# Kernel optimization log

Measured on AMD Instinct MI355X. Metric: run time of the kernel, lower is better.

Reference implementation:

```python
import jax, jax.numpy as jnp
import numpy as np

N, E, D, H, C = 50000, 800000, 128, 4, 32  # nodes, edges, embed dim, heads, head dim


def setup_inputs() -> dict:
    key = jax.random.key(0)
    ks = jax.random.split(key, 9)
    s = 1.0 / np.sqrt(D)
    return {
        "edge_index": jax.random.randint(ks[0], (2, E), 0, N),
        "emb": jax.random.normal(ks[1], (N, D), dtype=jnp.float32) * s,
        "W1": jax.random.normal(ks[2], (D, H * C), dtype=jnp.float32) * s,
        "att_src1": jax.random.normal(ks[3], (H, C), dtype=jnp.float32) * s,
        "att_dst1": jax.random.normal(ks[4], (H, C), dtype=jnp.float32) * s,
        "b1": jnp.zeros((H * C,), dtype=jnp.float32),
        "W2": jax.random.normal(ks[5], (D, D), dtype=jnp.float32) * s,
        "att_src2": jax.random.normal(ks[6], (1, D), dtype=jnp.float32) * s,
        "att_dst2": jax.random.normal(ks[7], (1, D), dtype=jnp.float32) * s,
        "b2": jnp.zeros((D,), dtype=jnp.float32),
    }


def _gat_conv(x, src, dst, W, a_src, a_dst, b, concat):
    """PyG-style GATConv: edge attention logits, segment softmax over dst, scatter-add."""
    n = x.shape[0]
    h, c = a_src.shape
    xl = (x @ W).reshape(n, h, c)                    # [N,H,C]
    a_s = (xl * a_src).sum(-1)                        # [N,H]
    a_d = (xl * a_dst).sum(-1)                        # [N,H]
    logits = jax.nn.leaky_relu(a_s[src] + a_d[dst], negative_slope=0.2)  # [E2,H]
    m = jax.ops.segment_max(logits, dst, num_segments=n)                 # per-dst max
    e = jnp.exp(logits - m[dst])
    denom = jax.ops.segment_sum(e, dst, num_segments=n)
    alpha = e / (denom[dst] + 1e-16)                  # [E2,H]
    msg = xl[src] * alpha[:, :, None]                 # [E2,H,C]
    out = jax.ops.segment_sum(msg, dst, num_segments=n)  # [N,H,C]
    out = out.reshape(n, h * c) if concat else out.mean(axis=1)
    return out + b


def reference(edge_index, emb, W1, att_src1, att_dst1, b1, W2, att_src2, att_dst2, b2):
    n = emb.shape[0]
    loop = jnp.arange(n)  # GATConv default add_self_loops=True
    src = jnp.concatenate([edge_index[0], loop])
    dst = jnp.concatenate([edge_index[1], loop])
    x = _gat_conv(emb, src, dst, W1, att_src1, att_dst1, b1, True)
    x = jax.nn.elu(x)
    x = _gat_conv(x, src, dst, W2, att_src2, att_dst2, b2, False)
    return x / jnp.maximum(jnp.linalg.norm(x, axis=1, keepdims=True), 1e-12)
```

## Files before the change

### kernel.cpp

```cpp
#include <hip/hip_runtime.h>
#include <hip/hip_bf16.h>
#include <math.h>

#define DD 128
#define CAP 64
#define NBKT 256
#define BCAP 5120
#define PCHUNK 4096
#define CSUB 8

typedef __attribute__((ext_vector_type(8))) short bf16x8;
typedef __attribute__((ext_vector_type(4))) float f32x4;

__device__ __forceinline__ float lrelu02(float x){ return x > 0.f ? x : 0.2f*x; }
__device__ __forceinline__ short f2bf(float f){
  __hip_bfloat16 h = __float2bfloat16(f);
  union { __hip_bfloat16 b; short s; } u; u.b = h; return u.s;
}

__global__ __launch_bounds__(256) void k_prep_hist(
    const float* __restrict__ W1, short* __restrict__ Wt1,
    const float* __restrict__ W2, short* __restrict__ Wt2,
    const int* __restrict__ dst, int* __restrict__ ghist, int E)
{
  __shared__ int hist[NBKT];
  int tid = threadIdx.x;
  hist[tid] = 0;
  int idx = blockIdx.x*256 + tid;
  if (idx < 2*DD*DD){
    const float* W = (idx < DD*DD) ? W1 : W2;
    short* Wt      = (idx < DD*DD) ? Wt1 : Wt2;
    int i2 = idx & (DD*DD - 1);
    int k = i2 >> 7, nn = i2 & 127;
    Wt[nn*DD + k] = f2bf(W[i2]);
  }
  __syncthreads();
  int e0 = blockIdx.x * PCHUNK;
  int e1 = min(e0 + PCHUNK, E);
  for (int e = e0 + tid; e < e1; e += 256)
    atomicAdd(&hist[dst[e] >> 8], 1);
  __syncthreads();
  if (e0 < E) ghist[blockIdx.x*NBKT + tid] = hist[tid];
}

__global__ __launch_bounds__(64) void k_scan(
    int* __restrict__ ghist, int* __restrict__ bcnt, int nblk)
{
  int b = blockIdx.x;
  int lane = threadIdx.x;
  int running = 0;
  for (int i0 = 0; i0 < nblk; i0 += 64){
    int i = i0 + lane;
    int v = (i < nblk) ? ghist[i*NBKT + b] : 0;
    int x = v;
    #pragma unroll
    for (int off = 1; off < 64; off <<= 1){
      int t = __shfl(x, lane - off, 64);
      if (lane >= off) x += t;
    }
    if (i < nblk) ghist[i*NBKT + b] = running + (x - v);
    running += __shfl(x, 63, 64);
  }
  if (lane == 0) bcnt[b] = running;
}

__global__ __launch_bounds__(256) void k_scatter2(
    const int* __restrict__ src, const int* __restrict__ dst,
    const int* __restrict__ ghist, unsigned int* __restrict__ part, int E)
{
  __shared__ int hist[NBKT];
  __shared__ int lb[NBKT];
  __shared__ int gb[NBKT];
  __shared__ unsigned int sdata[PCHUNK];
  __shared__ unsigned int saddr[PCHUNK];
  int tid = threadIdx.x;
  int e0 = blockIdx.x * PCHUNK;
  int e1 = min(e0 + PCHUNK, E);
  hist[tid] = 0;
  gb[tid] = ghist[blockIdx.x*NBKT + tid];
  __syncthreads();
  for (int e = e0 + tid; e < e1; e += 256)
    atomicAdd(&hist[dst[e] >> 8], 1);
  __syncthreads();
  if (tid < 64){
    int s0 = hist[4*tid], s1 = hist[4*tid+1], s2 = hist[4*tid+2], s3 = hist[4*tid+3];
    int s = s0 + s1 + s2 + s3;
    int x = s;
    #pragma unroll
    for (int off = 1; off < 64; off <<= 1){
      int t = __shfl(x, tid - off, 64);
      if (tid >= off) x += t;
    }
    int base = x - s;
    lb[4*tid]   = base;
    lb[4*tid+1] = base + s0;
    lb[4*tid+2] = base + s0 + s1;
    lb[4*tid+3] = base + s0 + s1 + s2;
  }
  __syncthreads();
  hist[tid] = 0;
  __syncthreads();
  for (int e = e0 + tid; e < e1; e += 256){
    int d = dst[e];
    int b = d >> 8;
    unsigned int pk = ((unsigned int)src[e] << 16) | (unsigned int)(d & 255);
    int pos = atomicAdd(&hist[b], 1);
    int loc = lb[b] + pos;
    int off = gb[b] + pos;
    sdata[loc] = pk;
    saddr[loc] = (off < BCAP) ? (unsigned int)(b*BCAP + off) : 0xFFFFFFFFu;
  }
  __syncthreads();
  int cn = e1 - e0;
  for (int t = tid; t < cn; t += 256){
    unsigned int a = saddr[t];
    if (a != 0xFFFFFFFFu) part[a] = sdata[t];
  }
}

__global__ __launch_bounds__(256) void k_csr(
    const int* __restrict__ bcnt, const unsigned int* __restrict__ part,
    int* __restrict__ cnt, unsigned short* __restrict__ csr, int N)
{
  __shared__ int cur[32];
  int b   = blockIdx.x >> 3;
  int sub = blockIdx.x & (CSUB-1);
  int nb = min(bcnt[b], BCAP);
  if (threadIdx.x < 32) cur[threadIdx.x] = 0;
  __syncthreads();
  const unsigned int* pb = part + (size_t)b*BCAP;
  for (int t = threadIdx.x; t < nb; t += 256){
    unsigned int pk = pb[t];
    int j = pk & 255;
    if ((j >> 5) == sub){
      int pos = atomicAdd(&cur[j & 31], 1);
      if (pos < CAP){
        int d = (b << 8) | j;
        csr[d*CAP + pos] = (unsigned short)(pk >> 16);
      }
    }
  }
  __syncthreads();
  if (threadIdx.x < 32){
    int d = (b << 8) | (sub << 5) | (int)threadIdx.x;
    if (d < N) cnt[d] = min(cur[threadIdx.x], CAP);
  }
}

template<int MODE>
__global__ __launch_bounds__(256) void k_gemm_mfma(
    const void* __restrict__ xin, const short* __restrict__ Wt,
    const float* __restrict__ att_s, const float* __restrict__ att_d,
    short* __restrict__ xl, float* __restrict__ as_, float* __restrict__ ad_, int n)
{
  __shared__ short Wl[DD*DD];
  {
    const float4* g = (const float4*)Wt;
    for (int c = threadIdx.x; c < DD*DD/8; c += 256){
      int row = c >> 4;
      int off = (c & 15) << 4;
      *(float4*)((char*)Wl + row*256 + (off ^ ((row&7)<<4))) = g[c];
    }
  }
  __syncthreads();

  const int lane = threadIdx.x & 63;
  const int wv   = threadIdx.x >> 6;
  const int col  = lane & 15;
  const int kg   = lane >> 4;
  const int row0 = blockIdx.x * 128;

  f32x4 acc[2][8];
  #pragma unroll
  for (int m=0;m<2;++m)
    #pragma unroll
    for (int t=0;t<8;++t) acc[m][t] = (f32x4){0.f,0.f,0.f,0.f};

  #pragma unroll
  for (int ks = 0; ks < 4; ++ks){
    bf16x8 afrag[2];
    #pragma unroll
    for (int m=0;m<2;++m){
      int r = row0 + wv*32 + m*16 + col;
      if (MODE == 0){
        bf16x8 a = (bf16x8)(short)0;
        if (r < n){
          const float* xf = (const float*)xin + (size_t)r*DD + ks*32 + kg*8;
          float4 fa = *(const float4*)xf;
          float4 fb = *(const float4*)(xf+4);
          a[0]=f2bf(fa.x); a[1]=f2bf(fa.y); a[2]=f2bf(fa.z); a[3]=f2bf(fa.w);
          a[4]=f2bf(fb.x); a[5]=f2bf(fb.y); a[6]=f2bf(fb.z); a[7]=f2bf(fb.w);
        }
        afrag[m] = a;
      } else {
        const short* xb = (const short*)xin + (size_t)r*DD + ks*32 + kg*8;
        afrag[m] = (r < n) ? *(const bf16x8*)xb : (bf16x8)(short)0;
      }
    }
    #pragma unroll
    for (int nt=0; nt<8; ++nt){
      int nrow = nt*16 + col;
      int koff = ks*64 + kg*16;
      bf16x8 b = *(const bf16x8*)((const char*)Wl + nrow*256 + (koff ^ ((nrow&7)<<4)));
      acc[0][nt] = __builtin_amdgcn_mfma_f32_16x16x32_bf16(afrag[0], b, acc[0][nt], 0,0,0);
      acc[1][nt] = __builtin_amdgcn_mfma_f32_16x16x32_bf16(afrag[1], b, acc[1][nt], 0,0,0);
    }
  }

  float ats[8], atd[8];
  #pragma unroll
  for (int nt=0;nt<8;++nt){ ats[nt]=att_s[nt*16+col]; atd[nt]=att_d[nt*16+col]; }

  #pragma unroll
  for (int m=0;m<2;++m){
    #pragma unroll
    for (int j=0;j<4;++j){
      int grow = row0 + wv*32 + m*16 + kg*4 + j;
      if (MODE==0){
        float ps[4]={0,0,0,0}, pd[4]={0,0,0,0};
        #pragma unroll
        for (int nt=0;nt<8;++nt){
          ps[nt>>1] += acc[m][nt][j]*ats[nt];
          pd[nt>>1] += acc[m][nt][j]*atd[nt];
        }
        #pragma unroll
        for (int h=0;h<4;++h){
          #pragma unroll
          for (int off=8; off; off>>=1){
            ps[h] += __shfl_xor(ps[h], off, 16);
            pd[h] += __shfl_xor(pd[h], off, 16);
          }
        }
        if (col==0 && grow<n){
          #pragma unroll
          for (int h=0;h<4;++h){ as_[grow*4+h]=ps[h]; ad_[grow*4+h]=pd[h]; }
        }
      } else {
        float ps=0, pd=0;
        #pragma unroll
        for (int nt=0;nt<8;++nt){ ps += acc[m][nt][j]*ats[nt]; pd += acc[m][nt][j]*atd[nt]; }
        #pragma unroll
        for (int off=8; off; off>>=1){
          ps += __shfl_xor(ps, off, 16);
          pd += __shfl_xor(pd, off, 16);
        }
        if (col==0 && grow<n){ as_[grow]=ps; ad_[grow]=pd; }
      }
    }
  }

  __syncthreads();
  #pragma unroll
  for (int m=0;m<2;++m)
    #pragma unroll
    for (int nt=0;nt<8;++nt)
      #pragma unroll
      for (int j=0;j<4;++j){
        int rl = wv*32 + m*16 + kg*4 + j;
        Wl[rl*DD + nt*16 + col] = f2bf(acc[m][nt][j]);
      }
  __syncthreads();
  {
    int rl = threadIdx.x >> 1;
    int grow = row0 + rl;
    if (grow < n){
      const float4* s = (const float4*)((const char*)Wl + rl*256 + (threadIdx.x&1)*128);
      float4* d = (float4*)((char*)xl + (size_t)grow*256 + (threadIdx.x&1)*128);
      #pragma unroll
      for (int q=0;q<8;++q) d[q]=s[q];
    }
  }
}

template<int HMODE>
__device__ __forceinline__ void agg_body(
    const unsigned int* __restrict__ xl, const float* __restrict__ as_,
    float adh, int lane, int h, int c, int b0, int n,
    const unsigned short* __restrict__ csr,
    float& a0, float& a1, float& den)
{
  const int jl = lane & 15;
  for (int e = 0; e < c; e += 16){
    int slot = min(e + jl, c - 1);
    int sw = csr[b0 + slot];
    float logit = (HMODE == 4) ? as_[sw*4 + h] : as_[sw];
    float wl = __expf(lrelu02(logit + adh));

    uint4 pk0 = *(const uint4*)(csr + b0 + e);
    uint4 pk1 = *(const uint4*)(csr + b0 + e + 8);
    unsigned int s16[16];
    s16[0]=pk0.x&0xffffu;  s16[1]=pk0.x>>16;  s16[2]=pk0.y&0xffffu;  s16[3]=pk0.y>>16;
    s16[4]=pk0.z&0xffffu;  s16[5]=pk0.z>>16;  s16[6]=pk0.w&0xffffu;  s16[7]=pk0.w>>16;
    s16[8]=pk1.x&0xffffu;  s16[9]=pk1.x>>16;  s16[10]=pk1.y&0xffffu; s16[11]=pk1.y>>16;
    s16[12]=pk1.z&0xffffu; s16[13]=pk1.z>>16; s16[14]=pk1.w&0xffffu; s16[15]=pk1.w>>16;

    if (e + 16 <= c){
      #pragma unroll
      for (int j = 0; j < 16; ++j){
        unsigned int v = xl[(size_t)s16[j]*64 + lane];
        float wj = __shfl(wl, (lane & 48) + j, 64);
        a0 += wj * __uint_as_float(v << 16);
        a1 += wj * __uint_as_float(v & 0xffff0000u);
        den += wj;
      }
    } else {
      int rem = c - e;
      #pragma unroll
      for (int j = 0; j < 16; ++j){
        unsigned int sj = min(s16[j], (unsigned int)(n - 1));
        unsigned int v = xl[(size_t)sj*64 + lane];
        float wj = __shfl(wl, (lane & 48) + j, 64);
        wj = (j < rem) ? wj : 0.f;
        a0 += wj * __uint_as_float(v << 16);
        a1 += wj * __uint_as_float(v & 0xffff0000u);
        den += wj;
      }
    }
  }
}

__global__ __launch_bounds__(256) void k_agg1(
    const unsigned int* __restrict__ xl, const float* __restrict__ as_,
    const float* __restrict__ ad_, const int* __restrict__ cnt,
    const unsigned short* __restrict__ csr,
    const float* __restrict__ b, unsigned int* __restrict__ out, int n)
{
  int wv = threadIdx.x >> 6, lane = threadIdx.x & 63;
  int i = blockIdx.x*4 + wv;
  if (i >= n) return;
  int h = lane >> 4;
  float adh = ad_[i*4+h];
  float wslf = __expf(lrelu02(as_[i*4+h] + adh));
  unsigned int xv = xl[(size_t)i*64 + lane];
  float a0 = wslf * __uint_as_float(xv << 16);
  float a1 = wslf * __uint_as_float(xv & 0xffff0000u);
  float den = wslf;
  int b0 = i*CAP;
  int c = min(cnt[i], CAP);

  agg_body<4>(xl, as_, adh, lane, h, c, b0, n, csr, a0, a1, den);

  float inv = 1.f/(den + 1e-16f);
  float o0 = a0*inv + b[2*lane];
  float o1 = a1*inv + b[2*lane+1];
  o0 = o0 > 0.f ? o0 : (__expf(o0)-1.f);
  o1 = o1 > 0.f ? o1 : (__expf(o1)-1.f);
  unsigned int p = ((unsigned int)(unsigned short)f2bf(o1) << 16) | (unsigned int)(unsigned short)f2bf(o0);
  out[(size_t)i*64 + lane] = p;
}

__global__ __launch_bounds__(256) void k_agg2(
    const unsigned int* __restrict__ xl, const float* __restrict__ as_,
    const float* __restrict__ ad_, const int* __restrict__ cnt,
    const unsigned short* __restrict__ csr,
    const float* __restrict__ b, float* __restrict__ out, int n)
{
  int wv = threadIdx.x >> 6, lane = threadIdx.x & 63;
  int i = blockIdx.x*4 + wv;
  if (i >= n) return;
  float adh = ad_[i];
  float wslf = __expf(lrelu02(as_[i] + adh));
  unsigned int xv = xl[(size_t)i*64 + lane];
  float a0 = wslf * __uint_as_float(xv << 16);
  float a1 = wslf * __uint_as_float(xv & 0xffff0000u);
  float den = wslf;
  int b0 = i*CAP;
  int c = min(cnt[i], CAP);

  agg_body<1>(xl, as_, adh, lane, 0, c, b0, n, csr, a0, a1, den);

  float inv = 1.f/(den + 1e-16f);
  float o0 = a0*inv + b[2*lane];
  float o1 = a1*inv + b[2*lane+1];
  float sq = o0*o0 + o1*o1;
  #pragma unroll
  for (int off = 32; off; off >>= 1) sq += __shfl_xor(sq, off, 64);
  float r = 1.f / fmaxf(sqrtf(sq), 1e-12f);
  ((float2*)(out + (size_t)i*DD))[lane] = make_float2(o0*r, o1*r);
}

extern "C" void kernel_launch(void* const* d_in, const int* in_sizes, int n_in,
                              void* d_out, int out_size, void* d_ws, size_t ws_size,
                              hipStream_t stream) {
  const int*   ei   = (const int*)d_in[0];
  const float* emb  = (const float*)d_in[1];
  const float* W1   = (const float*)d_in[2];
  const float* as1w = (const float*)d_in[3];
  const float* ad1w = (const float*)d_in[4];
  const float* b1   = (const float*)d_in[5];
  const float* W2   = (const float*)d_in[6];
  const float* as2w = (const float*)d_in[7];
  const float* ad2w = (const float*)d_in[8];
  const float* b2   = (const float*)d_in[9];
  const int E = in_sizes[0] / 2;
  const int N = in_sizes[1] / DD;
  const int* srcp = ei;
  const int* dstp = ei + E;
  const int nblk = (E + PCHUNK - 1) / PCHUNK;

  char* p = (char*)d_ws;
  auto alloc = [&](size_t bytes)->void*{
    void* r = (void*)p; p += (bytes + 255) & ~(size_t)255; return r;
  };
  int*            cntb  = (int*)alloc((size_t)N*4);
  int*            bcnt  = (int*)alloc((size_t)NBKT*4);
  int*            ghist = (int*)alloc((size_t)nblk*NBKT*4);
  unsigned int*   part  = (unsigned int*)alloc((size_t)NBKT*BCAP*4);
  unsigned short* csr   = (unsigned short*)alloc((size_t)N*CAP*2);
  short* Wt1    = (short*)alloc((size_t)DD*DD*2);
  short* Wt2    = (short*)alloc((size_t)DD*DD*2);
  short* xl1    = (short*)alloc((size_t)N*DD*2);
  short* x1     = (short*)alloc((size_t)N*DD*2);
  short* xl2    = (short*)alloc((size_t)N*DD*2);
  float* as1    = (float*)alloc((size_t)N*4*4);
  float* ad1    = (float*)alloc((size_t)N*4*4);
  float* as2    = (float*)alloc((size_t)N*4);
  float* ad2    = (float*)alloc((size_t)N*4);

  int nbk = (N + 255) / 256;
  int g1 = nblk > 2*DD*DD/256 ? nblk : 2*DD*DD/256;
  k_prep_hist<<<g1, 256, 0, stream>>>(W1, Wt1, W2, Wt2, dstp, ghist, E);
  k_scan     <<<NBKT, 64, 0, stream>>>(ghist, bcnt, nblk);
  k_scatter2 <<<nblk, 256, 0, stream>>>(srcp, dstp, ghist, part, E);
  k_csr      <<<nbk*CSUB, 256, 0, stream>>>(bcnt, part, cntb, csr, N);

  int gg = (N + 127) / 128;
  int gb = (N + 3) / 4;
  k_gemm_mfma<0><<<gg, 256, 0, stream>>>((const void*)emb, Wt1, as1w, ad1w, xl1, as1, ad1, N);
  k_agg1        <<<gb, 256, 0, stream>>>((const unsigned int*)xl1, as1, ad1, cntb, csr, b1, (unsigned int*)x1, N);
  k_gemm_mfma<1><<<gg, 256, 0, stream>>>((const void*)x1, Wt2, as2w, ad2w, xl2, as2, ad2, N);
  k_agg2        <<<gb, 256, 0, stream>>>((const unsigned int*)xl2, as2, ad2, cntb, csr, b2, (float*)d_out, N);
}
```

Measured before the change: 137.2 us.

## Merge CSR build and first GEMM into one launch; skip masked tail loads

The CSR bucket-fill kernel and the layer-1 MFMA GEMM are independent, so they now share one launch. The first blocks build the CSR and the rest run the GEMM, which removes one kernel launch and lets the two workloads overlap on the GPU. The CSR counters reuse the GEMM's shared-memory buffer, so every block reserves the full 32KB LDS, which may limit occupancy for the CSR blocks. Separately, the aggregation tail loop now uses a branch to skip out-of-range neighbors instead of clamping the index and zeroing the weight. This avoids redundant gathers but puts a shuffle inside divergent control flow.

```diff
diff --git a/kernel.cpp b/kernel.cpp
--- a/kernel.cpp
+++ b/kernel.cpp
@@ -118,42 +118,12 @@
   }
 }
 
-__global__ __launch_bounds__(256) void k_csr(
-    const int* __restrict__ bcnt, const unsigned int* __restrict__ part,
-    int* __restrict__ cnt, unsigned short* __restrict__ csr, int N)
-{
-  __shared__ int cur[32];
-  int b   = blockIdx.x >> 3;
-  int sub = blockIdx.x & (CSUB-1);
-  int nb = min(bcnt[b], BCAP);
-  if (threadIdx.x < 32) cur[threadIdx.x] = 0;
-  __syncthreads();
-  const unsigned int* pb = part + (size_t)b*BCAP;
-  for (int t = threadIdx.x; t < nb; t += 256){
-    unsigned int pk = pb[t];
-    int j = pk & 255;
-    if ((j >> 5) == sub){
-      int pos = atomicAdd(&cur[j & 31], 1);
-      if (pos < CAP){
-        int d = (b << 8) | j;
-        csr[d*CAP + pos] = (unsigned short)(pk >> 16);
-      }
-    }
-  }
-  __syncthreads();
-  if (threadIdx.x < 32){
-    int d = (b << 8) | (sub << 5) | (int)threadIdx.x;
-    if (d < N) cnt[d] = min(cur[threadIdx.x], CAP);
-  }
-}
-
 template<int MODE>
-__global__ __launch_bounds__(256) void k_gemm_mfma(
-    const void* __restrict__ xin, const short* __restrict__ Wt,
-    const float* __restrict__ att_s, const float* __restrict__ att_d,
-    short* __restrict__ xl, float* __restrict__ as_, float* __restrict__ ad_, int n)
-{
-  __shared__ short Wl[DD*DD];
+__device__ __forceinline__ void gemm_body(
+    short* Wl, const void* xin, const short* Wt,
+    const float* att_s, const float* att_d,
+    short* xl, float* as_, float* ad_, int n, int row0)
+{
   {
     const float4* g = (const float4*)Wt;
     for (int c = threadIdx.x; c < DD*DD/8; c += 256){
@@ -168,7 +138,6 @@
   const int wv   = threadIdx.x >> 6;
   const int col  = lane & 15;
   const int kg   = lane >> 4;
-  const int row0 = blockIdx.x * 128;
 
   f32x4 acc[2][8];
   #pragma unroll
@@ -272,6 +241,54 @@
   }
 }
 
+template<int MODE>
+__global__ __launch_bounds__(256) void k_gemm_mfma(
+    const void* __restrict__ xin, const short* __restrict__ Wt,
+    const float* __restrict__ att_s, const float* __restrict__ att_d,
+    short* __restrict__ xl, float* __restrict__ as_, float* __restrict__ ad_, int n)
+{
+  __shared__ short Wl[DD*DD];
+  gemm_body<MODE>(Wl, xin, Wt, att_s, att_d, xl, as_, ad_, n, blockIdx.x * 128);
+}
+
+__global__ __launch_bounds__(256) void k_csr_gemm(
+    const int* __restrict__ bcnt, const unsigned int* __restrict__ part,
+    int* __restrict__ cnt, unsigned short* __restrict__ csr, int N, int csrB,
+    const void* __restrict__ xin, const short* __restrict__ Wt,
+    const float* __restrict__ att_s, const float* __restrict__ att_d,
+    short* __restrict__ xl, float* __restrict__ as_, float* __restrict__ ad_)
+{
+  __shared__ short Wl[DD*DD];
+  if ((int)blockIdx.x < csrB){
+    int* cur = (int*)Wl;
+    int b   = blockIdx.x >> 3;
+    int sub = blockIdx.x & (CSUB-1);
+    int nb = min(bcnt[b], BCAP);
+    if (threadIdx.x < 32) cur[threadIdx.x] = 0;
+    __syncthreads();
+    const unsigned int* pb = part + (size_t)b*BCAP;
+    for (int t = threadIdx.x; t < nb; t += 256){
+      unsigned int pk = pb[t];
+      int j = pk & 255;
+      if ((j >> 5) == sub){
+        int pos = atomicAdd(&cur[j & 31], 1);
+        if (pos < CAP){
+          int d = (b << 8) | j;
+          csr[d*CAP + pos] = (unsigned short)(pk >> 16);
+        }
+      }
+    }
+    __syncthreads();
+    if (threadIdx.x < 32){
+      int d = (b << 8) | (sub << 5) | (int)threadIdx.x;
+      if (d < N) cnt[d] = min(cur[threadIdx.x], CAP);
+    }
+    return;
+  }
+  gemm_body<0>(Wl, xin, Wt, att_s, att_d, xl, as_, ad_, N,
+               ((int)blockIdx.x - csrB) * 128);
+}
+
 template<int HMODE>
 __device__ __forceinline__ void agg_body(
     const unsigned int* __restrict__ xl, const float* __restrict__ as_,
@@ -307,13 +324,13 @@
       int rem = c - e;
       #pragma unroll
       for (int j = 0; j < 16; ++j){
-        unsigned int sj = min(s16[j], (unsigned int)(n - 1));
-        unsigned int v = xl[(size_t)sj*64 + lane];
-        float wj = __shfl(wl, (lane & 48) + j, 64);
-        wj = (j < rem) ? wj : 0.f;
-        a0 += wj * __uint_as_float(v << 16);
-        a1 += wj * __uint_as_float(v & 0xffff0000u);
-        den += wj;
+        if (j < rem){
+          unsigned int v = xl[(size_t)s16[j]*64 + lane];
+          float wj = __shfl(wl, (lane & 48) + j, 64);
+          a0 += wj * __uint_as_float(v << 16);
+          a1 += wj * __uint_as_float(v & 0xffff0000u);
+          den += wj;
+        }
       }
     }
   }
@@ -418,15 +435,17 @@
   float* ad2    = (float*)alloc((size_t)N*4);
 
   int nbk = (N + 255) / 256;
+  int csrB = nbk * CSUB;
+  int gg = (N + 127) / 128;
+  int gb = (N + 3) / 4;
   int g1 = nblk > 2*DD*DD/256 ? nblk : 2*DD*DD/256;
+
   k_prep_hist<<<g1, 256, 0, stream>>>(W1, Wt1, W2, Wt2, dstp, ghist, E);
   k_scan     <<<NBKT, 64, 0, stream>>>(ghist, bcnt, nblk);
   k_scatter2 <<<nblk, 256, 0, stream>>>(srcp, dstp, ghist, part, E);
-  k_csr      <<<nbk*CSUB, 256, 0, stream>>>(bcnt, part, cntb, csr, N);
-
-  int gg = (N + 127) / 128;
-  int gb = (N + 3) / 4;
-  k_gemm_mfma<0><<<gg, 256, 0, stream>>>((const void*)emb, Wt1, as1w, ad1w, xl1, as1, ad1, N);
+  k_csr_gemm <<<csrB + gg, 256, 0, stream>>>(bcnt, part, cntb, csr, N, csrB,
+                                             (const void*)emb, Wt1, as1w, ad1w,
+                                             xl1, as1, ad1);
   k_agg1        <<<gb, 256, 0, stream>>>((const unsigned int*)xl1, as1, ad1, cntb, csr, b1, (unsigned int*)x1, N);
   k_gemm_mfma<1><<<gg, 256, 0, stream>>>((const void*)x1, Wt2, as2w, ad2w, xl2, as2, ad2, N);
   k_agg2        <<<gb, 256, 0, stream>>>((const unsigned int*)xl2, as2, ad2, cntb, csr, b2, (float*)d_out, N);
```

New measurement: 164.1 us. +19.7%, slower.
